# Optimization experiments

Hardware: AMD Instinct MI355X
Metric: run time of the kernel (lower is better)

The kernel has to match this reference:

```python
import jax, jax.numpy as jnp
import numpy as np

WX, WY = 32, 32
N = WX * WY                      # 1024 tokens
TOKEN_DIM = 1024
QKV = 512
H = 8
HD = QKV // H                    # 64
TOPK = 32
B = 64
NUM_UNIQUE = (2 * WX - 1) * (2 * WY - 1)  # 3969 unique relative offsets
LN_EPS = 1e-5


def _make_rel_idx():
    # identical to torch create_positional_biases: lexicographic unique index of (dx, dy)
    ix = np.arange(N) // WY
    iy = np.arange(N) % WY
    dx = ix[:, None] - ix[None, :]
    dy = iy[:, None] - iy[None, :]
    rel = (dx + WX - 1) * (2 * WY - 1) + (dy + WY - 1)
    return jnp.asarray(rel, dtype=jnp.int32)  # [N, N]


def _layernorm(x, g, b):
    m = jnp.mean(x, axis=-1, keepdims=True)
    v = jnp.mean(jnp.square(x - m), axis=-1, keepdims=True)
    return (x - m) * jax.lax.rsqrt(v + LN_EPS) * g + b


def setup_inputs() -> dict:
    key = jax.random.key(0)
    ks = jax.random.split(key, 12)
    s = 0.02
    return {
        "x": jax.random.normal(ks[0], (B, N, TOKEN_DIM), jnp.float32),
        "scorer_w": jax.random.normal(ks[1], (1, TOKEN_DIM), jnp.float32) * s,
        "scorer_b": jnp.zeros((1,), jnp.float32),
        "ln_g": jnp.ones((TOKEN_DIM,), jnp.float32),
        "ln_b": jnp.zeros((TOKEN_DIM,), jnp.float32),
        "qk_w": jax.random.normal(ks[2], (QKV, TOKEN_DIM), jnp.float32) * s,
        "qk_b": jnp.zeros((QKV,), jnp.float32),
        "v_w": jax.random.normal(ks[3], (QKV, TOKEN_DIM), jnp.float32) * s,
        "v_b": jnp.zeros((QKV,), jnp.float32),
        "skip_w": jax.random.normal(ks[4], (QKV, TOKEN_DIM), jnp.float32) * s,
        "skip_b": jnp.zeros((QKV,), jnp.float32),
        "out_w": jax.random.normal(ks[5], (QKV, QKV), jnp.float32) * s,
        "out_b": jnp.zeros((QKV,), jnp.float32),
        "fc_w": jax.random.normal(ks[6], (2, QKV), jnp.float32) * s,
        "fc_b": jnp.zeros((2,), jnp.float32),
        "unique_bias": jax.random.normal(ks[7], (NUM_UNIQUE,), jnp.float32) * s,
        "rel_idx": _make_rel_idx(),
    }


def reference(x, scorer_w, scorer_b, ln_g, ln_b, qk_w, qk_b, v_w, v_b,
              skip_w, skip_b, out_w, out_b, fc_w, fc_b, unique_bias, rel_idx):
    # token selection (eval path: argmax of relevance logits)
    logits = jnp.einsum('bnd,od->bno', x, scorer_w)[..., 0] + scorer_b[0]  # [B, N]
    sel_idx = jnp.argmax(logits, axis=-1)                                   # [B]
    sel_tok = x[jnp.arange(B), sel_idx]                                     # [B, D]

    x_n = _layernorm(x, ln_g, ln_b)
    s_n = _layernorm(sel_tok, ln_g, ln_b)

    value = (jnp.einsum('bnd,qd->bnq', x_n, v_w) + v_b).reshape(B, N, H, HD).transpose(0, 2, 1, 3)  # [B,H,N,hd]
    key_t = (jnp.einsum('bnd,qd->bnq', x_n, qk_w) + qk_b).reshape(B, N, H, HD).transpose(0, 2, 1, 3)
    query = (s_n @ qk_w.T + qk_b).reshape(B, H, HD)                         # [B,H,hd]

    attn = jnp.einsum('bhd,bhnd->bhn', query, key_t) / jnp.sqrt(jnp.float32(HD))  # [B,H,N]
    bias = unique_bias[rel_idx[sel_idx]]                                    # gather: [B, N]
    attn = jax.nn.softmax(attn + bias[:, None, :], axis=-1)

    # top-k sparsification + renormalization
    _, topk_idx = jax.lax.top_k(attn, TOPK)                                 # [B,H,K]
    mask = jax.nn.one_hot(topk_idx, N, dtype=attn.dtype).sum(axis=-2)       # [B,H,N] 0/1
    attn = attn * mask
    attn = attn / (attn.sum(axis=-1, keepdims=True) + 1e-9)

    y = jnp.einsum('bhn,bhnd->bhd', attn, value).reshape(B, QKV)            # [B, QKV]
    skip = sel_tok @ skip_w.T + skip_b
    y = jax.nn.relu(y + skip)
    # dropout is identity in eval mode
    y = y @ out_w.T + out_b
    y = y @ fc_w.T + fc_b
    return y  # [B, 2]
```

## Files before the change

kernel.cpp:

```cpp
#include <hip/hip_runtime.h>
#include <hip/hip_bf16.h>
#include <math.h>

#define WX 32
#define WY 32
#define NTOK 1024
#define TD 1024
#define QKV 512
#define NH 8
#define HD 64
#define TOPK 32
#define BB 64

__device__ __forceinline__ float wred_sum(float v){
  #pragma unroll
  for (int o=32;o;o>>=1) v += __shfl_xor(v,o,64);
  return v;
}
__device__ __forceinline__ float wred_max(float v){
  #pragma unroll
  for (int o=32;o;o>>=1) v = fmaxf(v, __shfl_xor(v,o,64));
  return v;
}
__device__ __forceinline__ float dot4f(float4 a, float4 b){
  return a.x*b.x + a.y*b.y + a.z*b.z + a.w*b.w;
}

__global__ __launch_bounds__(256) void k1_stats(
    const float* __restrict__ x, const float* __restrict__ sw, const float* __restrict__ sb,
    float* __restrict__ mean, float* __restrict__ rstd, float* __restrict__ logit){
  int wave = threadIdx.x >> 6, lane = threadIdx.x & 63;
  int tok = blockIdx.x*4 + wave;
  const float4* xp = (const float4*)(x + (size_t)tok*TD);
  const float4* sp = (const float4*)sw;
  float s1=0.f, s2=0.f, sd=0.f;
  #pragma unroll
  for (int j=0;j<4;j++){
    float4 v = xp[lane + j*64];
    float4 w = sp[lane + j*64];
    s1 += v.x+v.y+v.z+v.w;
    s2 += v.x*v.x + v.y*v.y + v.z*v.z + v.w*v.w;
    sd += dot4f(v,w);
  }
  s1 = wred_sum(s1); s2 = wred_sum(s2); sd = wred_sum(sd);
  if (lane==0){
    float m = s1*(1.f/1024.f);
    float var = s2*(1.f/1024.f) - m*m;
    mean[tok] = m;
    rstd[tok] = rsqrtf(var + 1e-5f);
    logit[tok] = sd + sb[0];
  }
}

__global__ __launch_bounds__(256) void k2_prep(
    const float* __restrict__ x, const float* __restrict__ logit,
    const float* __restrict__ mean, const float* __restrict__ rstd,
    const float* __restrict__ lng, const float* __restrict__ lnb,
    const float* __restrict__ qkw, const float* __restrict__ qkb,
    const int* __restrict__ relIdx, const float* __restrict__ ub,
    int* __restrict__ selI, float* __restrict__ gu8,
    float* __restrict__ Aw, float* __restrict__ C0w, float* __restrict__ biasArr){
  __shared__ float sn[TD];
  __shared__ float qs[HD];
  __shared__ float red[256];
  __shared__ float redV[4]; __shared__ int redI[4];
  __shared__ int sel_s;
  int b = blockIdx.x >> 3, h = blockIdx.x & 7;
  int t = threadIdx.x, lane = t&63, wave = t>>6;

  const float* lg = logit + b*NTOK;
  float bv = -INFINITY; int bi = 0;
  #pragma unroll
  for (int j=0;j<4;j++){ int idx = t*4+j; float v = lg[idx]; if (v > bv){ bv=v; bi=idx; } }
  #pragma unroll
  for (int o=32;o;o>>=1){
    float vv = __shfl_xor(bv,o,64); int ii = __shfl_xor(bi,o,64);
    if (vv > bv || (vv == bv && ii < bi)){ bv=vv; bi=ii; }
  }
  if (lane==0){ redV[wave]=bv; redI[wave]=bi; }
  __syncthreads();
  if (t==0){
    float v = redV[0]; int i = redI[0];
    for (int w=1; w<4; w++){ if (redV[w] > v || (redV[w]==v && redI[w]<i)){ v=redV[w]; i=redI[w]; } }
    sel_s = i;
    if (h==0) selI[b] = i;
  }
  __syncthreads();
  int sel = sel_s;
  float m = mean[b*NTOK+sel], r = rstd[b*NTOK+sel];
  float4 g4 = ((const float4*)lng)[t];
  float4 b4 = ((const float4*)lnb)[t];
  {
    float4 xv = ((const float4*)(x + ((size_t)b*NTOK + sel)*TD))[t];
    float4 s4;
    s4.x = (xv.x-m)*r*g4.x + b4.x;
    s4.y = (xv.y-m)*r*g4.y + b4.y;
    s4.z = (xv.z-m)*r*g4.z + b4.z;
    s4.w = (xv.w-m)*r*g4.w + b4.w;
    ((float4*)sn)[t] = s4;
  }
  __syncthreads();
  {
    int row = t>>2, part = t&3;
    const float4* wr = (const float4*)(qkw + (size_t)(h*HD+row)*TD + part*256);
    const float4* xp = ((const float4*)sn) + part*64;
    float a0 = 0.f, a1 = 0.f;
    #pragma unroll 4
    for (int j=0;j<64;j+=2){ a0 += dot4f(wr[j], xp[j]); a1 += dot4f(wr[j+1], xp[j+1]); }
    red[t] = a0 + a1;
  }
  __syncthreads();
  if (t < HD) qs[t] = red[t*4]+red[t*4+1]+red[t*4+2]+red[t*4+3] + qkb[h*HD+t];
  __syncthreads();
  float4 accE = make_float4(0.f,0.f,0.f,0.f);
  float4 accO = make_float4(0.f,0.f,0.f,0.f);
  #pragma unroll 4
  for (int c=0;c<HD;c+=2){
    float q0 = qs[c], q1 = qs[c+1];
    float4 w0 = ((const float4*)(qkw + (size_t)(h*HD+c)*TD))[t];
    float4 w1 = ((const float4*)(qkw + (size_t)(h*HD+c+1)*TD))[t];
    accE.x += q0*w0.x; accE.y += q0*w0.y; accE.z += q0*w0.z; accE.w += q0*w0.w;
    accO.x += q1*w1.x; accO.y += q1*w1.y; accO.z += q1*w1.z; accO.w += q1*w1.w;
  }
  float4 acc;
  acc.x = accE.x+accO.x; acc.y = accE.y+accO.y; acc.z = accE.z+accO.z; acc.w = accE.w+accO.w;
  {
    float4 gu;
    gu.x = acc.x*g4.x*0.125f; gu.y = acc.y*g4.y*0.125f;
    gu.z = acc.z*g4.z*0.125f; gu.w = acc.w*g4.w*0.125f;
    ((float4*)(gu8 + ((size_t)(b*NH+h))*TD))[t] = gu;
  }
  float su_p = g4.x*acc.x + g4.y*acc.y + g4.z*acc.z + g4.w*acc.w;
  float bu_p = b4.x*acc.x + b4.y*acc.y + b4.z*acc.z + b4.w*acc.w;
  su_p = wred_sum(su_p); bu_p = wred_sum(bu_p);
  if (lane==0){ red[wave] = su_p; red[8+wave] = bu_p; }
  if (wave==0){
    float qb_p = qs[lane]*qkb[h*HD+lane];
    qb_p = wred_sum(qb_p);
    if (lane==0) red[16] = qb_p;
  }
  __syncthreads();
  if (t==0){
    float s  = red[0]+red[1]+red[2]+red[3];
    float bb = red[8]+red[9]+red[10]+red[11];
    Aw[b*NH+h]  = s*0.125f;
    C0w[b*NH+h] = (bb + red[16])*0.125f;
  }
  if (h==0){
    const int* rp = relIdx + (size_t)sel*NTOK;
    #pragma unroll
    for (int j=0;j<4;j++){
      int n = t*4+j;
      biasArr[b*NTOK+n] = ub[rp[n]];
    }
  }
}

__global__ __launch_bounds__(256) void k3_attn(
    const float* __restrict__ x, const float* __restrict__ mean, const float* __restrict__ rstd,
    const float* __restrict__ gu8, const float* __restrict__ Aw, const float* __restrict__ C0w,
    const float* __restrict__ biasArr, float* __restrict__ attL){
  int b = blockIdx.x >> 4;
  int chunk = blockIdx.x & 15;
  int lane = threadIdx.x & 63, wave = threadIdx.x >> 6;

  const float4* gp = (const float4*)(gu8 + (size_t)b*NH*TD);
  float4 G[NH][4];
  #pragma unroll
  for (int h=0;h<NH;h++)
    #pragma unroll
    for (int j=0;j<4;j++)
      G[h][j] = gp[h*256 + j*64 + lane];
  float Ah[NH], Ch[NH];
  #pragma unroll
  for (int h=0;h<NH;h++){ Ah[h] = Aw[b*NH+h]; Ch[h] = C0w[b*NH+h]; }

  const int base = chunk*64 + wave*16;
  float4 cur[4];
  {
    const float4* xp = (const float4*)(x + ((size_t)b*NTOK + base)*TD);
    #pragma unroll
    for (int j=0;j<4;j++) cur[j] = xp[j*64 + lane];
  }
  for (int i=0;i<16;i++){
    int n = base + i;
    int tok = b*NTOK + n;
    float4 nxt[4];
    if (i < 15){
      const float4* xp = (const float4*)(x + (size_t)(tok+1)*TD);
      #pragma unroll
      for (int j=0;j<4;j++) nxt[j] = xp[j*64 + lane];
    }
    float m = mean[tok], r = rstd[tok], bias = biasArr[b*NTOK+n];
    float s[NH];
    #pragma unroll
    for (int h=0;h<NH;h++){
      float a = dot4f(cur[0],G[h][0]) + dot4f(cur[1],G[h][1])
              + dot4f(cur[2],G[h][2]) + dot4f(cur[3],G[h][3]);
      s[h] = wred_sum(a);
    }
    #pragma unroll
    for (int h=0;h<NH;h++){
      if (lane == h)
        attL[((size_t)b*NH+h)*NTOK + n] = r*s[h] - r*m*Ah[h] + Ch[h] + bias;
    }
    if (i < 15){
      #pragma unroll
      for (int j=0;j<4;j++) cur[j] = nxt[j];
    }
  }
}

__global__ __launch_bounds__(256) void k4_topkv(
    const float* __restrict__ x, const float* __restrict__ mean, const float* __restrict__ rstd,
    const float* __restrict__ lng, const float* __restrict__ lnb,
    const float* __restrict__ vw, const float* __restrict__ vb,
    const float* __restrict__ attL, const int* __restrict__ selI,
    const float* __restrict__ skw, const float* __restrict__ skb,
    float* __restrict__ t1ws){
  __shared__ float redf[4];
  __shared__ float cV[128]; __shared__ int cI[128];
  __shared__ float selV[TOPK]; __shared__ int selIs[TOPK];
  __shared__ float aa[TOPK]; __shared__ float am[TOPK];
  __shared__ float xbar[TD];
  __shared__ float red2[256];
  int b = blockIdx.x >> 3, h = blockIdx.x & 7;
  int t = threadIdx.x, lane = t&63, wave = t>>6;

  float4 Lv = ((const float4*)(attL + ((size_t)b*NH + h)*NTOK))[t];
  float lm = fmaxf(fmaxf(Lv.x,Lv.y), fmaxf(Lv.z,Lv.w));
  lm = wred_max(lm);
  if (lane==0) redf[wave] = lm;
  __syncthreads();
  float maxL = fmaxf(fmaxf(redf[0],redf[1]), fmaxf(redf[2],redf[3]));
  __syncthreads();
  float ev[4];
  ev[0] = __expf(Lv.x - maxL); ev[1] = __expf(Lv.y - maxL);
  ev[2] = __expf(Lv.z - maxL); ev[3] = __expf(Lv.w - maxL);
  float zp = ev[0]+ev[1]+ev[2]+ev[3];
  zp = wred_sum(zp);
  if (lane==0) redf[wave] = zp;
  __syncthreads();
  float Z = redf[0]+redf[1]+redf[2]+redf[3];

  for (int k=0;k<TOPK;k++){
    float bv = -1.f; int bi = 1<<20;
    #pragma unroll
    for (int j=0;j<4;j++){ if (ev[j] > bv){ bv = ev[j]; bi = t*4+j; } }
    #pragma unroll
    for (int o=32;o;o>>=1){
      float vv = __shfl_xor(bv,o,64); int ii = __shfl_xor(bi,o,64);
      if (vv > bv || (vv == bv && ii < bi)){ bv=vv; bi=ii; }
    }
    #pragma unroll
    for (int j=0;j<4;j++){ if (bi == t*4+j) ev[j] = -1.f; }
    if (lane==0){ cV[wave*TOPK+k] = bv; cI[wave*TOPK+k] = bi; }
  }
  __syncthreads();
  float selContrib = 0.f;
  if (t < 128){
    float v = cV[t]; int idx = cI[t];
    int rank = 0;
    #pragma unroll 8
    for (int j0=0;j0<32;j0++){
      float4 v4 = ((float4*)cV)[j0];
      int4  i4 = ((int4*)cI)[j0];
      rank += (v4.x > v) || (v4.x==v && i4.x<idx);
      rank += (v4.y > v) || (v4.y==v && i4.y<idx);
      rank += (v4.z > v) || (v4.z==v && i4.z<idx);
      rank += (v4.w > v) || (v4.w==v && i4.w<idx);
    }
    if (rank < TOPK){ selV[rank]=v; selIs[rank]=idx; selContrib = v; }
  }
  float Sp = wred_sum(selContrib);
  if (lane==0) redf[wave] = Sp;
  __syncthreads();
  float S = redf[0]+redf[1]+redf[2]+redf[3];
  float denom = S + 1e-9f*Z;
  float W = S/denom;
  if (t < TOPK){
    int ni = selIs[t];
    float w = selV[t]/denom;
    float a = w * rstd[b*NTOK+ni];
    aa[t] = a; am[t] = a*mean[b*NTOK+ni];
  }
  __syncthreads();
  float c = 0.f;
  #pragma unroll
  for (int k=0;k<TOPK;k++) c += am[k];

  float4 acc = make_float4(0.f,0.f,0.f,0.f);
  for (int k=0;k<TOPK;k++){
    float a = aa[k];
    float4 xv = ((const float4*)(x + ((size_t)b*NTOK + selIs[k])*TD))[t];
    acc.x += a*xv.x; acc.y += a*xv.y; acc.z += a*xv.z; acc.w += a*xv.w;
  }
  float4 g4 = ((const float4*)lng)[t];
  float4 b4 = ((const float4*)lnb)[t];
  float4 xb;
  xb.x = g4.x*(acc.x - c) + b4.x*W;
  xb.y = g4.y*(acc.y - c) + b4.y*W;
  xb.z = g4.z*(acc.z - c) + b4.z*W;
  xb.w = g4.w*(acc.w - c) + b4.w*W;
  ((float4*)xbar)[t] = xb;
  __syncthreads();

  int co = t >> 2, part = t & 3;
  int row = h*HD + co;
  {
    const float4* vp = (const float4*)(vw + (size_t)row*TD + part*256);
    const float4* xp2 = ((const float4*)xbar) + part*64;
    float a0 = 0.f, a1 = 0.f;
    #pragma unroll 4
    for (int j=0;j<64;j+=2){ a0 += dot4f(vp[j], xp2[j]); a1 += dot4f(vp[j+1], xp2[j+1]); }
    red2[t] = a0 + a1;
  }
  int sel = selI[b];
  float4 xs4 = ((const float4*)(x + ((size_t)b*NTOK + sel)*TD))[t];
  __syncthreads();
  float ypart = 0.f;
  if (part==0) ypart = red2[t]+red2[t+1]+red2[t+2]+red2[t+3] + vb[row]*W;
  ((float4*)xbar)[t] = xs4;
  __syncthreads();
  {
    const float4* wr = (const float4*)(skw + (size_t)row*TD + part*256);
    const float4* xp2 = ((const float4*)xbar) + part*64;
    float a0 = 0.f, a1 = 0.f;
    #pragma unroll 4
    for (int j=0;j<64;j+=2){ a0 += dot4f(wr[j], xp2[j]); a1 += dot4f(wr[j+1], xp2[j+1]); }
    red2[t] = a0 + a1;
  }
  __syncthreads();
  if (part==0){
    float skip = red2[t]+red2[t+1]+red2[t+2]+red2[t+3] + skb[row];
    t1ws[b*QKV + row] = fmaxf(ypart + skip, 0.f);
  }
}

__global__ __launch_bounds__(256) void k5bc(
    const float* __restrict__ t1ws, const float* __restrict__ ow,
    const float* __restrict__ ob, const float* __restrict__ fcw,
    const float* __restrict__ fcb, float* __restrict__ out){
  __shared__ float t1s[QKV];
  __shared__ float t2s[QKV];
  __shared__ float redA[4]; __shared__ float redB[4];
  int b = blockIdx.x, t = threadIdx.x, lane = t&63, wave = t>>6;
  if (t < 128) ((float4*)t1s)[t] = ((const float4*)(t1ws + (size_t)b*QKV))[t];
  __syncthreads();
  int r0 = 2*t;
  {
    const float4* w0 = (const float4*)(ow + (size_t)r0*QKV);
    const float4* w1 = (const float4*)(ow + (size_t)(r0+1)*QKV);
    float a0 = 0.f, a1 = 0.f;
    #pragma unroll 8
    for (int j=0;j<128;j++){ float4 x4 = ((float4*)t1s)[j]; a0 += dot4f(w0[j], x4); a1 += dot4f(w1[j], x4); }
    t2s[r0]   = a0 + ob[r0];
    t2s[r0+1] = a1 + ob[r0+1];
  }
  __syncthreads();
  float v0 = t2s[r0], v1 = t2s[r0+1];
  float p0 = v0*fcw[r0] + v1*fcw[r0+1];
  float p1 = v0*fcw[QKV+r0] + v1*fcw[QKV+r0+1];
  p0 = wred_sum(p0); p1 = wred_sum(p1);
  if (lane==0){ redA[wave]=p0; redB[wave]=p1; }
  __syncthreads();
  if (t==0){
    out[b*2+0] = redA[0]+redA[1]+redA[2]+redA[3] + fcb[0];
    out[b*2+1] = redB[0]+redB[1]+redB[2]+redB[3] + fcb[1];
  }
}

extern "C" void kernel_launch(void* const* d_in, const int* in_sizes, int n_in,
                              void* d_out, int out_size, void* d_ws, size_t ws_size,
                              hipStream_t stream) {
  const float* x   = (const float*)d_in[0];
  const float* sw  = (const float*)d_in[1];
  const float* sb  = (const float*)d_in[2];
  const float* lng = (const float*)d_in[3];
  const float* lnb = (const float*)d_in[4];
  const float* qkw = (const float*)d_in[5];
  const float* qkb = (const float*)d_in[6];
  const float* vw  = (const float*)d_in[7];
  const float* vb  = (const float*)d_in[8];
  const float* skw = (const float*)d_in[9];
  const float* skb = (const float*)d_in[10];
  const float* ow  = (const float*)d_in[11];
  const float* ob  = (const float*)d_in[12];
  const float* fcw = (const float*)d_in[13];
  const float* fcb = (const float*)d_in[14];
  const float* ub  = (const float*)d_in[15];
  const int*   ri  = (const int*)d_in[16];
  float* out = (float*)d_out;

  float* wsf     = (float*)d_ws;
  float* logit   = wsf;
  float* mean    = wsf + 65536;
  float* rstd    = wsf + 131072;
  int*   selI    = (int*)(wsf + 196608);
  float* gu8     = wsf + 196672;
  float* Aw      = wsf + 720960;
  float* C0w     = wsf + 721472;
  float* biasArr = wsf + 721984;
  float* attL    = wsf + 787520;
  float* t1ws    = wsf + 1311808;

  k1_stats<<<16384, 256, 0, stream>>>(x, sw, sb, mean, rstd, logit);
  k2_prep<<<BB*NH, 256, 0, stream>>>(x, logit, mean, rstd, lng, lnb, qkw, qkb,
                                     ri, ub, selI, gu8, Aw, C0w, biasArr);
  k3_attn<<<BB*16, 256, 0, stream>>>(x, mean, rstd, gu8, Aw, C0w, biasArr, attL);
  k4_topkv<<<BB*NH, 256, 0, stream>>>(x, mean, rstd, lng, lnb, vw, vb, attL,
                                      selI, skw, skb, t1ws);
  k5bc<<<BB, 256, 0, stream>>>(t1ws, ow, ob, fcw, fcb, out);
}
```

Baseline: 577.0 us.

## Fuse argmax into stats via atomicMax, stage attL stores, fuse output MLP

Token-selection argmax moves into k1_stats. Each block packs an order-preserving float key with the reversed token index, so ties go to the lowest index, and issues a 64-bit atomicMax per batch. This removes the per-block logit scan that k2 repeated eight times per batch. k3 now stages attention logits in shared memory and writes them back coalesced per head instead of using scattered single-lane stores. The final out/fc kernel is folded into k4 with a last-block-done counter, which needs an added memset of the workspace and threadfence ordering.

```diff
diff --git a/kernel.cpp b/kernel.cpp
--- a/kernel.cpp
+++ b/kernel.cpp
@@ -25,12 +25,19 @@
 __device__ __forceinline__ float dot4f(float4 a, float4 b){
   return a.x*b.x + a.y*b.y + a.z*b.z + a.w*b.w;
 }
+__device__ __forceinline__ unsigned int f2ord(float f){
+  unsigned int u = __float_as_uint(f);
+  return (u & 0x80000000u) ? ~u : (u | 0x80000000u);
+}
 
 __global__ __launch_bounds__(256) void k1_stats(
     const float* __restrict__ x, const float* __restrict__ sw, const float* __restrict__ sb,
-    float* __restrict__ mean, float* __restrict__ rstd, float* __restrict__ logit){
+    float* __restrict__ mean, float* __restrict__ rstd,
+    unsigned long long* __restrict__ packed){
+  __shared__ unsigned long long keys[4];
   int wave = threadIdx.x >> 6, lane = threadIdx.x & 63;
   int tok = blockIdx.x*4 + wave;
+  int b = blockIdx.x >> 8;
   const float4* xp = (const float4*)(x + (size_t)tok*TD);
   const float4* sp = (const float4*)sw;
   float s1=0.f, s2=0.f, sd=0.f;
@@ -48,12 +55,22 @@
     float var = s2*(1.f/1024.f) - m*m;
     mean[tok] = m;
     rstd[tok] = rsqrtf(var + 1e-5f);
-    logit[tok] = sd + sb[0];
+    float logit = sd + sb[0];
+    int n = tok & (NTOK-1);
+    keys[wave] = ((unsigned long long)f2ord(logit) << 10) | (unsigned long long)(NTOK-1-n);
+  }
+  __syncthreads();
+  if (threadIdx.x==0){
+    unsigned long long k = keys[0];
+    if (keys[1] > k) k = keys[1];
+    if (keys[2] > k) k = keys[2];
+    if (keys[3] > k) k = keys[3];
+    atomicMax(&packed[b], k);
   }
 }
 
 __global__ __launch_bounds__(256) void k2_prep(
-    const float* __restrict__ x, const float* __restrict__ logit,
+    const float* __restrict__ x, const unsigned long long* __restrict__ packed,
     const float* __restrict__ mean, const float* __restrict__ rstd,
     const float* __restrict__ lng, const float* __restrict__ lnb,
     const float* __restrict__ qkw, const float* __restrict__ qkb,
@@ -63,30 +80,11 @@
   __shared__ float sn[TD];
   __shared__ float qs[HD];
   __shared__ float red[256];
-  __shared__ float redV[4]; __shared__ int redI[4];
-  __shared__ int sel_s;
   int b = blockIdx.x >> 3, h = blockIdx.x & 7;
   int t = threadIdx.x, lane = t&63, wave = t>>6;
 
-  const float* lg = logit + b*NTOK;
-  float bv = -INFINITY; int bi = 0;
-  #pragma unroll
-  for (int j=0;j<4;j++){ int idx = t*4+j; float v = lg[idx]; if (v > bv){ bv=v; bi=idx; } }
-  #pragma unroll
-  for (int o=32;o;o>>=1){
-    float vv = __shfl_xor(bv,o,64); int ii = __shfl_xor(bi,o,64);
-    if (vv > bv || (vv == bv && ii < bi)){ bv=vv; bi=ii; }
-  }
-  if (lane==0){ redV[wave]=bv; redI[wave]=bi; }
-  __syncthreads();
-  if (t==0){
-    float v = redV[0]; int i = redI[0];
-    for (int w=1; w<4; w++){ if (redV[w] > v || (redV[w]==v && redI[w]<i)){ v=redV[w]; i=redI[w]; } }
-    sel_s = i;
-    if (h==0) selI[b] = i;
-  }
-  __syncthreads();
-  int sel = sel_s;
+  int sel = NTOK-1 - (int)(packed[b] & (NTOK-1));
+  if (h==0 && t==0) selI[b] = sel;
   float m = mean[b*NTOK+sel], r = rstd[b*NTOK+sel];
   float4 g4 = ((const float4*)lng)[t];
   float4 b4 = ((const float4*)lnb)[t];
@@ -160,6 +158,7 @@
     const float* __restrict__ x, const float* __restrict__ mean, const float* __restrict__ rstd,
     const float* __restrict__ gu8, const float* __restrict__ Aw, const float* __restrict__ C0w,
     const float* __restrict__ biasArr, float* __restrict__ attL){
+  __shared__ float sL[NH*65];
   int b = blockIdx.x >> 4;
   int chunk = blockIdx.x & 15;
   int lane = threadIdx.x & 63, wave = threadIdx.x >> 6;
@@ -202,12 +201,18 @@
     #pragma unroll
     for (int h=0;h<NH;h++){
       if (lane == h)
-        attL[((size_t)b*NH+h)*NTOK + n] = r*s[h] - r*m*Ah[h] + Ch[h] + bias;
+        sL[h*65 + wave*16 + i] = r*s[h] - r*m*Ah[h] + Ch[h] + bias;
     }
     if (i < 15){
       #pragma unroll
       for (int j=0;j<4;j++) cur[j] = nxt[j];
     }
+  }
+  __syncthreads();
+  #pragma unroll
+  for (int hh=0; hh<2; hh++){
+    int h = wave + hh*4;
+    attL[((size_t)b*NH+h)*NTOK + chunk*64 + lane] = sL[h*65 + lane];
   }
 }
 
@@ -217,13 +222,18 @@
     const float* __restrict__ vw, const float* __restrict__ vb,
     const float* __restrict__ attL, const int* __restrict__ selI,
     const float* __restrict__ skw, const float* __restrict__ skb,
-    float* __restrict__ t1ws){
+    float* __restrict__ t1ws, int* __restrict__ cnt,
+    const float* __restrict__ ow, const float* __restrict__ ob,
+    const float* __restrict__ fcw, const float* __restrict__ fcb,
+    float* __restrict__ out){
   __shared__ float redf[4];
   __shared__ float cV[128]; __shared__ int cI[128];
   __shared__ float selV[TOPK]; __shared__ int selIs[TOPK];
   __shared__ float aa[TOPK]; __shared__ float am[TOPK];
   __shared__ float xbar[TD];
   __shared__ float red2[256];
+  __shared__ int lastFlag;
+  __shared__ float redA[4]; __shared__ float redB[4];
   int b = blockIdx.x >> 3, h = blockIdx.x & 7;
   int t = threadIdx.x, lane = t&63, wave = t>>6;
 
@@ -335,16 +345,16 @@
     float skip = red2[t]+red2[t+1]+red2[t+2]+red2[t+3] + skb[row];
     t1ws[b*QKV + row] = fmaxf(ypart + skip, 0.f);
   }
-}
-
-__global__ __launch_bounds__(256) void k5bc(
-    const float* __restrict__ t1ws, const float* __restrict__ ow,
-    const float* __restrict__ ob, const float* __restrict__ fcw,
-    const float* __restrict__ fcb, float* __restrict__ out){
-  __shared__ float t1s[QKV];
-  __shared__ float t2s[QKV];
-  __shared__ float redA[4]; __shared__ float redB[4];
-  int b = blockIdx.x, t = threadIdx.x, lane = t&63, wave = t>>6;
+  __syncthreads();
+  if (t==0){
+    __threadfence();
+    lastFlag = (atomicAdd(&cnt[b], 1) == NH-1);
+  }
+  __syncthreads();
+  if (!lastFlag) return;
+  __threadfence();
+  float* t1s = xbar;
+  float* t2s = xbar + QKV;
   if (t < 128) ((float4*)t1s)[t] = ((const float4*)(t1ws + (size_t)b*QKV))[t];
   __syncthreads();
   int r0 = 2*t;
@@ -392,23 +402,25 @@
   const int*   ri  = (const int*)d_in[16];
   float* out = (float*)d_out;
 
-  float* wsf     = (float*)d_ws;
-  float* logit   = wsf;
-  float* mean    = wsf + 65536;
-  float* rstd    = wsf + 131072;
-  int*   selI    = (int*)(wsf + 196608);
-  float* gu8     = wsf + 196672;
-  float* Aw      = wsf + 720960;
-  float* C0w     = wsf + 721472;
-  float* biasArr = wsf + 721984;
-  float* attL    = wsf + 787520;
-  float* t1ws    = wsf + 1311808;
-
-  k1_stats<<<16384, 256, 0, stream>>>(x, sw, sb, mean, rstd, logit);
-  k2_prep<<<BB*NH, 256, 0, stream>>>(x, logit, mean, rstd, lng, lnb, qkw, qkb,
+  float* wsf = (float*)d_ws;
+  unsigned long long* packed = (unsigned long long*)d_ws;
+  int*   cnt     = (int*)(wsf + 128);
+  float* mean    = wsf + 256;
+  float* rstd    = wsf + 65792;
+  int*   selI    = (int*)(wsf + 131328);
+  float* gu8     = wsf + 131392;
+  float* Aw      = wsf + 655680;
+  float* C0w     = wsf + 656192;
+  float* biasArr = wsf + 656704;
+  float* attL    = wsf + 722240;
+  float* t1ws    = wsf + 1246528;
+
+  hipMemsetAsync(d_ws, 0, 1024, stream);
+  k1_stats<<<16384, 256, 0, stream>>>(x, sw, sb, mean, rstd, packed);
+  k2_prep<<<BB*NH, 256, 0, stream>>>(x, packed, mean, rstd, lng, lnb, qkw, qkb,
                                      ri, ub, selI, gu8, Aw, C0w, biasArr);
   k3_attn<<<BB*16, 256, 0, stream>>>(x, mean, rstd, gu8, Aw, C0w, biasArr, attL);
   k4_topkv<<<BB*NH, 256, 0, stream>>>(x, mean, rstd, lng, lnb, vw, vb, attL,
-                                      selI, skw, skb, t1ws);
-  k5bc<<<BB, 256, 0, stream>>>(t1ws, ow, ob, fcw, fcb, out);
-}
+                                      selI, skw, skb, t1ws, cnt,
+                                      ow, ob, fcw, fcb, out);
+}
```

New measurement: 624.1 us. +8.2%, slower.
